# Optimization experiments

Measured on AMD Instinct MI355X. Metric: run time of the kernel, lower is better.

Reference implementation:

```python
import jax, jax.numpy as jnp
import numpy as np
import math

B, S, D, H, N = 4, 2048, 1024, 8, 128  # batch, seq_len, d_model, n_heads, num_osc
ITERS = 10
DT = 0.1
PI = math.pi


def setup_inputs() -> dict:
    key = jax.random.key(0)
    ks = jax.random.split(key, 5)
    return {
        "x": jax.random.normal(ks[0], (B, S, D), jnp.float32),
        "mask": jnp.ones((B, S), jnp.int32),
        "W_phase": jax.random.normal(ks[1], (D, H * N), jnp.float32) / math.sqrt(D),
        "b_phase": jnp.zeros((H * N,), jnp.float32),
        "natural_freq": jax.random.normal(ks[2], (H, N), jnp.float32) * 0.1,
        "coupling": jnp.ones((H, 1, 1), jnp.float32),  # coupling_strength = 1.0
        "W_out": jax.random.normal(ks[3], (H * N, D), jnp.float32) / math.sqrt(H * N),
        "b_out": jnp.zeros((D,), jnp.float32),
    }


def reference(x, mask, W_phase, b_phase, natural_freq, coupling, W_out, b_out):
    # phases: [B, H, S, N]
    ph = (x @ W_phase + b_phase).reshape(B, S, H, N).transpose(0, 2, 1, 3)
    ph = jnp.tanh(ph) * PI
    m = mask.astype(ph.dtype)[:, None, :, None]  # [B,1,S,1] mask over j
    K = coupling.reshape(1, H, 1, 1)
    w = natural_freq.reshape(1, H, 1, N)

    def step(ph, _):
        s = jnp.sin(ph)
        c = jnp.cos(ph)
        # mean_j m_j * sin(theta_i - theta_j) = sin(th_i)*mean(m*cos) - cos(th_i)*mean(m*sin)
        ms = (m * s).mean(axis=2, keepdims=True)  # [B,H,1,N]
        mc = (m * c).mean(axis=2, keepdims=True)
        dtheta = w + K * (s * mc - c * ms)
        ph2 = jnp.mod(ph + DT * dtheta + PI, 2 * PI) - PI
        return ph2, None

    ph, _ = jax.lax.scan(step, ph, None, length=ITERS)
    # from_phase; dropout is identity in eval mode
    y = ph.transpose(0, 2, 1, 3).reshape(B, S, H * N) @ W_out + b_out
    return y
```

## Files before the change

### kernel.cpp

```cpp
#include <hip/hip_runtime.h>
#include <math.h>

#define S_ 2048
#define D_ 1024
#define HN_ 1024
#define B_ 4
#define M_ 8192
#define ITERS_ 10
#define DT_ 0.1f
#define PI_ 3.14159265358979323846f
#define TWOPI_ 6.28318530717958647692f
#define INV2PI_ 0.15915494309189533577f
#define SCALE_ 4096.0f
#define INVSC2_ (1.0f / 16777216.0f)

typedef __attribute__((ext_vector_type(8))) _Float16 f16x8;
typedef __attribute__((ext_vector_type(4))) float f32x4;

__device__ __align__(16) ushort g_xs [(size_t)M_ * 2048];
__device__ __align__(16) ushort g_WpT[(size_t)HN_ * 2048];
__device__ __align__(16) ushort g_WoT[(size_t)D_ * 1024];
__device__ __align__(16) float  g_ph [(size_t)B_ * HN_ * S_];
__device__ __align__(16) ushort g_phh[(size_t)B_ * HN_ * S_];
__device__ __align__(16) ushort g_phT[(size_t)M_ * HN_];

__device__ __forceinline__ ushort f2h(float f) {
    union { _Float16 h; ushort u; } v; v.h = (_Float16)f; return v.u;
}
__device__ __forceinline__ void split2s(float x, ushort& A, ushort& Bc) {
    const float xs = x * SCALE_;
    union { _Float16 h; ushort u; } va, vb;
    va.h = (_Float16)xs;
    const float r = xs - (float)va.h;
    vb.h = (_Float16)r;
    A = va.u; Bc = vb.u;
}
__device__ __forceinline__ void gload16(const void* g, void* l) {
    __builtin_amdgcn_global_load_lds(
        (const __attribute__((address_space(1))) void*)g,
        (__attribute__((address_space(3))) void*)l, 16, 0, 0);
}
__device__ __forceinline__ int pack2(ushort a, ushort b) {
    return (int)(unsigned)a | ((int)(unsigned)b << 16);
}

__global__ __launch_bounds__(256) void split_x(const float* __restrict__ X) {
    const int idx = blockIdx.x * 256 + threadIdx.x;
    const float4 v = ((const float4*)X)[idx];
    const int m  = idx >> 8;
    const int k4 = (idx & 255) * 4;
    ushort a[4], b[4];
    split2s(v.x, a[0], b[0]);
    split2s(v.y, a[1], b[1]);
    split2s(v.z, a[2], b[2]);
    split2s(v.w, a[3], b[3]);
    ushort* row = g_xs + (size_t)m * 2048 + k4;
    int2 oa; oa.x = pack2(a[0], a[1]); oa.y = pack2(a[2], a[3]);
    int2 ob; ob.x = pack2(b[0], b[1]); ob.y = pack2(b[2], b[3]);
    *(int2*)(row)        = oa;
    *(int2*)(row + 1024) = ob;
}

__global__ __launch_bounds__(256) void splitT_Wp(const float* __restrict__ Wp) {
    __shared__ float t[64][68];
    const int k0 = blockIdx.x * 64;
    const int n0 = blockIdx.y * 64;
    const int r = threadIdx.x >> 2;
    const int c = (threadIdx.x & 3) * 16;
    const float* src = Wp + (size_t)(k0 + r) * HN_ + n0 + c;
    #pragma unroll
    for (int q = 0; q < 4; ++q)
        *(float4*)&t[r][c + 4 * q] = ((const float4*)src)[q];
    __syncthreads();
    ushort ha[16], hb[16];
    #pragma unroll
    for (int j = 0; j < 16; ++j)
        split2s(t[c + j][r], ha[j], hb[j]);
    int4 a0, a1, b0, b1;
    a0.x = pack2(ha[0], ha[1]);   a0.y = pack2(ha[2], ha[3]);
    a0.z = pack2(ha[4], ha[5]);   a0.w = pack2(ha[6], ha[7]);
    a1.x = pack2(ha[8], ha[9]);   a1.y = pack2(ha[10], ha[11]);
    a1.z = pack2(ha[12], ha[13]); a1.w = pack2(ha[14], ha[15]);
    b0.x = pack2(hb[0], hb[1]);   b0.y = pack2(hb[2], hb[3]);
    b0.z = pack2(hb[4], hb[5]);   b0.w = pack2(hb[6], hb[7]);
    b1.x = pack2(hb[8], hb[9]);   b1.y = pack2(hb[10], hb[11]);
    b1.z = pack2(hb[12], hb[13]); b1.w = pack2(hb[14], hb[15]);
    ushort* dst = g_WpT + (size_t)(n0 + r) * 2048 + k0 + c;
    *(int4*)(dst)        = a0; *(int4*)(dst + 8)    = a1;
    *(int4*)(dst + 1024) = b0; *(int4*)(dst + 1032) = b1;
}

__global__ __launch_bounds__(256) void castT_Wo(const float* __restrict__ Wo) {
    __shared__ float t[64][68];
    const int k0 = blockIdx.x * 64;
    const int n0 = blockIdx.y * 64;
    const int r = threadIdx.x >> 2;
    const int c = (threadIdx.x & 3) * 16;
    const float* src = Wo + (size_t)(k0 + r) * D_ + n0 + c;
    #pragma unroll
    for (int q = 0; q < 4; ++q)
        *(float4*)&t[r][c + 4 * q] = ((const float4*)src)[q];
    __syncthreads();
    ushort h[16];
    #pragma unroll
    for (int j = 0; j < 16; ++j) h[j] = f2h(t[c + j][r]);
    ushort* dst = g_WoT + (size_t)(n0 + r) * 1024 + k0 + c;
    int4 o0, o1;
    o0.x = pack2(h[0], h[1]);   o0.y = pack2(h[2], h[3]);
    o0.z = pack2(h[4], h[5]);   o0.w = pack2(h[6], h[7]);
    o1.x = pack2(h[8], h[9]);   o1.y = pack2(h[10], h[11]);
    o1.z = pack2(h[12], h[13]); o1.w = pack2(h[14], h[15]);
    *(int4*)dst = o0;
    *(int4*)(dst + 8) = o1;
}

template<int NT, int SPLIT>
__device__ __forceinline__ void gemm_mainloop(const ushort* __restrict__ A,
                                              const ushort* __restrict__ Bm,
                                              ushort* lds,
                                              int m0, int n0, int tid,
                                              f32x4 (&acc)[4][4]) {
    constexpr int KROW = SPLIT ? 2048 : 1024;
    const int l   = tid & 63, wid = tid >> 6;
    const int wm  = wid >> 1, wn = wid & 1;
    const int l15 = l & 15, h = l >> 4;
    const int row4 = tid >> 2;
    const int soff = ((tid & 3) ^ (row4 & 3)) << 4;
    const char* gA = (const char*)(A + (size_t)m0 * KROW);
    const char* gB = (const char*)(Bm + (size_t)n0 * KROW);
    const int rdA = (wm * 64 + l15) * 64 + ((h ^ (l15 & 3)) << 4);
    const int rdB = 8192 + (wn * 64 + l15) * 64 + ((h ^ (l15 & 3)) << 4);

    #define AOFF(T) ((SPLIT && (T) >= 64) ? 2048 + ((T) - 64) * 64 : ((T) & 31) * 64)
    #define BOFF(T) (SPLIT ? ((T) < 32 ? (T) * 64 : ((T) < 64 ? 2048 + ((T) - 32) * 64 \
                                                              : ((T) - 64) * 64)) : (T) * 64)

    #define STAGE(T, BUF) do {                                                    \
        const int ao_ = AOFF(T), bo_ = BOFF(T);                                   \
        char* lb_ = (char*)lds + (BUF) * 16384;                                   \
        gload16(gA + (size_t)(row4)      * (KROW * 2) + ao_ + soff, lb_ + tid * 16);          \
        gload16(gA + (size_t)(row4 + 64) * (KROW * 2) + ao_ + soff, lb_ + 4096 + tid * 16);   \
        gload16(gB + (size_t)(row4)      * (KROW * 2) + bo_ + soff, lb_ + 8192 + tid * 16);   \
        gload16(gB + (size_t)(row4 + 64) * (KROW * 2) + bo_ + soff, lb_ + 12288 + tid * 16);  \
    } while (0)

    #define SB __builtin_amdgcn_sched_barrier(0)

    STAGE(0, 0);

    #pragma unroll 2
    for (int t = 0; t < NT; ++t) {
        SB; __builtin_amdgcn_s_barrier(); SB;
        if (t + 1 < NT) {
            STAGE(t + 1, (t + 1) & 1);
            asm volatile("s_waitcnt vmcnt(4)" ::: "memory");
        } else {
            asm volatile("s_waitcnt vmcnt(0)" ::: "memory");
        }
        SB; __builtin_amdgcn_s_barrier(); SB;

        const char* bb = (const char*)lds + (t & 1) * 16384;
        f16x8 Aa[4], Bb[4];
        #pragma unroll
        for (int i = 0; i < 4; ++i) Aa[i] = *(const f16x8*)(bb + rdA + i * 1024);
        #pragma unroll
        for (int j = 0; j < 4; ++j) Bb[j] = *(const f16x8*)(bb + rdB + j * 1024);
        __builtin_amdgcn_s_setprio(1);
        #pragma unroll
        for (int i = 0; i < 4; ++i)
            #pragma unroll
            for (int j = 0; j < 4; ++j)
                acc[i][j] = __builtin_amdgcn_mfma_f32_16x16x32_f16(
                    Aa[i], Bb[j], acc[i][j], 0, 0, 0);
        __builtin_amdgcn_s_setprio(0);
    }
    #undef STAGE
    #undef SB
    #undef AOFF
    #undef BOFF
}

__device__ __forceinline__ void tile_map(int bid, int& m0, int& n0) {
    const int xcd = bid & 7;
    const int idx = bid >> 3;
    m0 = (xcd * 8 + (idx >> 3)) * 128;
    n0 = (idx & 7) * 128;
}

__global__ __launch_bounds__(256, 4) void gemm1(const float* __restrict__ bias) {
    __shared__ ushort lds[2 * 8192];
    const int tid = threadIdx.x;
    int m0, n0;
    tile_map(blockIdx.x, m0, n0);
    const int wid = tid >> 6, l = tid & 63;
    const int wm = wid >> 1, wn = wid & 1;

    f32x4 acc[4][4];
    #pragma unroll
    for (int i = 0; i < 4; ++i)
        #pragma unroll
        for (int j = 0; j < 4; ++j) acc[i][j] = (f32x4){0.f, 0.f, 0.f, 0.f};

    gemm_mainloop<96, 1>(g_xs, g_WpT, lds, m0, n0, tid, acc);

    const int r4 = (l >> 4) * 4;
    const int cn = l & 15;
    #pragma unroll
    for (int i = 0; i < 4; ++i) {
        const int mg = m0 + wm * 64 + i * 16 + r4;
        const int bidx = mg >> 11;
        const int sg = mg & 2047;
        #pragma unroll
        for (int jj = 0; jj < 4; ++jj) {
            const int ng = n0 + wn * 64 + jj * 16 + cn;
            const float bb = bias[ng];
            float4 o;
            o.x = PI_ * tanhf(fmaf(acc[i][jj][0], INVSC2_, bb));
            o.y = PI_ * tanhf(fmaf(acc[i][jj][1], INVSC2_, bb));
            o.z = PI_ * tanhf(fmaf(acc[i][jj][2], INVSC2_, bb));
            o.w = PI_ * tanhf(fmaf(acc[i][jj][3], INVSC2_, bb));
            *(float4*)(g_ph + ((size_t)bidx * HN_ + ng) * S_ + sg) = o;
        }
    }
}

__global__ __launch_bounds__(256, 4) void gemm3(const float* __restrict__ bias,
                                                float* __restrict__ Y) {
    __shared__ ushort lds[2 * 8192];
    const int tid = threadIdx.x;
    int m0, n0;
    tile_map(blockIdx.x, m0, n0);
    const int wid = tid >> 6, l = tid & 63;
    const int wm = wid >> 1, wn = wid & 1;

    f32x4 acc[4][4];
    #pragma unroll
    for (int i = 0; i < 4; ++i)
        #pragma unroll
        for (int j = 0; j < 4; ++j) acc[i][j] = (f32x4){0.f, 0.f, 0.f, 0.f};

    gemm_mainloop<32, 0>(g_phT, g_WoT, lds, m0, n0, tid, acc);

    const int r4 = (l >> 4) * 4;
    const int cn = l & 15;
    #pragma unroll
    for (int i = 0; i < 4; ++i) {
        const int mg = m0 + wm * 64 + i * 16 + r4;
        #pragma unroll
        for (int jj = 0; jj < 4; ++jj) {
            const int ng = n0 + wn * 64 + jj * 16 + cn;
            const float bb = bias[ng];
            #pragma unroll
            for (int r = 0; r < 4; ++r)
                Y[(size_t)(mg + r) * D_ + ng] = acc[i][jj][r] + bb;
        }
    }
}

__global__ __launch_bounds__(256) void kuramoto(const int* __restrict__ mask,
                                                const float* __restrict__ natf,
                                                const float* __restrict__ coup) {
    const int wave = blockIdx.x * 4 + (threadIdx.x >> 6);
    const int lane = threadIdx.x & 63;
    const int b = wave >> 10;
    const int hn = wave & 1023;
    const int h = hn >> 7;

    const float wf = natf[hn];
    const float K = coup[h];

    const float* base = g_ph + ((size_t)b * HN_ + hn) * S_;

    float ph[32];
    #pragma unroll
    for (int i = 0; i < 8; ++i) {
        float4 v = *(const float4*)(base + i * 256 + lane * 4);
        ph[4 * i + 0] = v.x; ph[4 * i + 1] = v.y;
        ph[4 * i + 2] = v.z; ph[4 * i + 3] = v.w;
    }

    const int* mb = mask + b * S_;
    unsigned mbits = 0;
    #pragma unroll
    for (int i = 0; i < 8; ++i) {
        int4 mv = *(const int4*)(mb + i * 256 + lane * 4);
        mbits |= (mv.x != 0 ? 1u : 0u) << (4 * i + 0);
        mbits |= (mv.y != 0 ? 1u : 0u) << (4 * i + 1);
        mbits |= (mv.z != 0 ? 1u : 0u) << (4 * i + 2);
        mbits |= (mv.w != 0 ? 1u : 0u) << (4 * i + 3);
    }

    for (int it = 0; it < ITERS_; ++it) {
        float s[32], c[32];
        float ls = 0.f, lc = 0.f;
        #pragma unroll
        for (int i = 0; i < 32; ++i) {
            s[i] = __sinf(ph[i]);
            c[i] = __cosf(ph[i]);
            const float mf = (float)((mbits >> i) & 1u);
            ls = fmaf(mf, s[i], ls);
            lc = fmaf(mf, c[i], lc);
        }
        #pragma unroll
        for (int off = 32; off; off >>= 1) {
            ls += __shfl_xor(ls, off);
            lc += __shfl_xor(lc, off);
        }
        const float ms = ls * (1.f / 2048.f);
        const float mc = lc * (1.f / 2048.f);
        #pragma unroll
        for (int i = 0; i < 32; ++i) {
            const float dth = fmaf(K, fmaf(s[i], mc, -c[i] * ms), wf);
            float t = fmaf(DT_, dth, ph[i]) + PI_;
            t -= TWOPI_ * floorf(t * INV2PI_);
            ph[i] = t - PI_;
        }
    }

    ushort* ob = g_phh + ((size_t)b * HN_ + hn) * S_;
    #pragma unroll
    for (int i = 0; i < 8; ++i) {
        ushort4 o;
        o.x = f2h(ph[4 * i + 0]); o.y = f2h(ph[4 * i + 1]);
        o.z = f2h(ph[4 * i + 2]); o.w = f2h(ph[4 * i + 3]);
        *(ushort4*)(ob + i * 256 + lane * 4) = o;
    }
}

__global__ __launch_bounds__(256) void transpose_ph() {
    __shared__ ushort t[64][72];
    const int b = blockIdx.z;
    const int h0 = blockIdx.y * 64;
    const int s0 = blockIdx.x * 64;
    const int r = threadIdx.x >> 2;
    const int c = (threadIdx.x & 3) * 16;
    const ushort* src = g_phh + ((size_t)b * HN_ + h0 + r) * S_ + s0 + c;
    *(int4*)&t[r][c] = *(const int4*)src;
    *(int4*)&t[r][c + 8] = *(const int4*)(src + 8);
    __syncthreads();
    ushort o[16];
    #pragma unroll
    for (int j = 0; j < 16; ++j) o[j] = t[c + j][r];
    ushort* dst = g_phT + ((size_t)(b * S_ + s0 + r)) * HN_ + h0 + c;
    int4 o0, o1;
    o0.x = pack2(o[0], o[1]);   o0.y = pack2(o[2], o[3]);
    o0.z = pack2(o[4], o[5]);   o0.w = pack2(o[6], o[7]);
    o1.x = pack2(o[8], o[9]);   o1.y = pack2(o[10], o[11]);
    o1.z = pack2(o[12], o[13]); o1.w = pack2(o[14], o[15]);
    *(int4*)dst = o0;
    *(int4*)(dst + 8) = o1;
}

extern "C" void kernel_launch(void* const* d_in, const int* in_sizes, int n_in,
                              void* d_out, int out_size, void* d_ws, size_t ws_size,
                              hipStream_t stream) {
    const float* x    = (const float*)d_in[0];
    const int*   mask = (const int*)d_in[1];
    const float* Wp   = (const float*)d_in[2];
    const float* bp   = (const float*)d_in[3];
    const float* natf = (const float*)d_in[4];
    const float* coup = (const float*)d_in[5];
    const float* Wo   = (const float*)d_in[6];
    const float* bo   = (const float*)d_in[7];
    float* y = (float*)d_out;

    split_x  <<<dim3(8192),         256, 0, stream>>>(x);
    splitT_Wp<<<dim3(16, 16),       256, 0, stream>>>(Wp);
    castT_Wo <<<dim3(16, 16),       256, 0, stream>>>(Wo);
    gemm1    <<<dim3(512),          256, 0, stream>>>(bp);
    kuramoto <<<dim3(1024),         256, 0, stream>>>(mask, natf, coup);
    transpose_ph<<<dim3(32, 16, 4), 256, 0, stream>>>();
    gemm3    <<<dim3(512),          256, 0, stream>>>(bo, y);
}
```

Before: 192.6 us.

## Retile GEMMs to 128x64 blocks with 8 waves and 64-wide K stages

Both GEMM kernels move from 128x128 tiles with 4 waves (each wave computing 64x64) to 128x64 tiles with 8 waves (each wave computing 32x32). Each stage now loads a K-slice of 64 instead of 32, with a new XOR swizzle for shared memory, and the launch grids double to 1024 blocks of 512 threads. The goal is more waves and blocks in flight to raise occupancy and hide latency. In exchange each wave gets less register-level reuse, and B tiles are reloaded more often across the grid.

```diff
diff --git a/kernel.cpp b/kernel.cpp
--- a/kernel.cpp
+++ b/kernel.cpp
@@ -119,29 +119,38 @@
                                               const ushort* __restrict__ Bm,
                                               ushort* lds,
                                               int m0, int n0, int tid,
-                                              f32x4 (&acc)[4][4]) {
+                                              f32x4 (&acc)[2][2]) {
     constexpr int KROW = SPLIT ? 2048 : 1024;
-    const int l   = tid & 63, wid = tid >> 6;
-    const int wm  = wid >> 1, wn = wid & 1;
-    const int l15 = l & 15, h = l >> 4;
-    const int row4 = tid >> 2;
-    const int soff = ((tid & 3) ^ (row4 & 3)) << 4;
+    const int l = tid & 63, wid = tid >> 6;
+    const int wm = wid >> 1, wn = wid & 1;
+    const int r8   = l >> 3;
+    const int swzo = ((l & 7) * 16) ^ (r8 << 4);
     const char* gA = (const char*)(A + (size_t)m0 * KROW);
     const char* gB = (const char*)(Bm + (size_t)n0 * KROW);
-    const int rdA = (wm * 64 + l15) * 64 + ((h ^ (l15 & 3)) << 4);
-    const int rdB = 8192 + (wn * 64 + l15) * 64 + ((h ^ (l15 & 3)) << 4);
-
-    #define AOFF(T) ((SPLIT && (T) >= 64) ? 2048 + ((T) - 64) * 64 : ((T) & 31) * 64)
-    #define BOFF(T) (SPLIT ? ((T) < 32 ? (T) * 64 : ((T) < 64 ? 2048 + ((T) - 32) * 64 \
-                                                              : ((T) - 64) * 64)) : (T) * 64)
-
-    #define STAGE(T, BUF) do {                                                    \
-        const int ao_ = AOFF(T), bo_ = BOFF(T);                                   \
-        char* lb_ = (char*)lds + (BUF) * 16384;                                   \
-        gload16(gA + (size_t)(row4)      * (KROW * 2) + ao_ + soff, lb_ + tid * 16);          \
-        gload16(gA + (size_t)(row4 + 64) * (KROW * 2) + ao_ + soff, lb_ + 4096 + tid * 16);   \
-        gload16(gB + (size_t)(row4)      * (KROW * 2) + bo_ + soff, lb_ + 8192 + tid * 16);   \
-        gload16(gB + (size_t)(row4 + 64) * (KROW * 2) + bo_ + soff, lb_ + 12288 + tid * 16);  \
+
+    const int l15 = l & 15;
+    const int xk  = (l15 & 7) << 4;
+    const int sl0 = (((l >> 4) * 16)) ^ xk;
+    const int sl1 = (64 + ((l >> 4) * 16)) ^ xk;
+    const char* pA = (const char*)lds + (wm * 32 + l15) * 128;
+    const char* pB = (const char*)lds + 16384 + (wn * 32 + l15) * 128;
+
+    #define AOFF(T) ((size_t)(SPLIT ? ((T) < 32 ? ((T) & 15) * 128 : 2048 + ((T) - 32) * 128) \
+                                    : (T) * 128))
+    #define BOFF(T) ((size_t)(SPLIT ? ((T) < 16 ? (T) * 128                                   \
+                                     : ((T) < 32 ? 2048 + ((T) - 16) * 128                    \
+                                                 : ((T) - 32) * 128))                         \
+                                    : (T) * 128))
+
+    #define STAGE(T, BUF) do {                                                     \
+        const size_t ao_ = AOFF(T) + swzo, bo_ = BOFF(T) + swzo;                   \
+        char* lb_ = (char*)lds + (BUF) * 24576;                                    \
+        gload16(gA + (size_t)(wid * 16 + r8)     * (KROW * 2) + ao_,               \
+                lb_ + wid * 2048);                                                 \
+        gload16(gA + (size_t)(wid * 16 + 8 + r8) * (KROW * 2) + ao_,               \
+                lb_ + wid * 2048 + 1024);                                          \
+        gload16(gB + (size_t)(wid * 8 + r8)      * (KROW * 2) + bo_,               \
+                lb_ + 16384 + wid * 1024);                                         \
     } while (0)
 
     #define SB __builtin_amdgcn_sched_barrier(0)
@@ -153,25 +162,33 @@
         SB; __builtin_amdgcn_s_barrier(); SB;
         if (t + 1 < NT) {
             STAGE(t + 1, (t + 1) & 1);
-            asm volatile("s_waitcnt vmcnt(4)" ::: "memory");
+            asm volatile("s_waitcnt vmcnt(3)" ::: "memory");
         } else {
             asm volatile("s_waitcnt vmcnt(0)" ::: "memory");
         }
         SB; __builtin_amdgcn_s_barrier(); SB;
 
-        const char* bb = (const char*)lds + (t & 1) * 16384;
-        f16x8 Aa[4], Bb[4];
-        #pragma unroll
-        for (int i = 0; i < 4; ++i) Aa[i] = *(const f16x8*)(bb + rdA + i * 1024);
-        #pragma unroll
-        for (int j = 0; j < 4; ++j) Bb[j] = *(const f16x8*)(bb + rdB + j * 1024);
+        const int bo = (t & 1) * 24576;
+        f16x8 Aa[2][2], Bb[2][2];
+        #pragma unroll
+        for (int i = 0; i < 2; ++i) {
+            Aa[i][0] = *(const f16x8*)(pA + bo + i * 2048 + sl0);
+            Aa[i][1] = *(const f16x8*)(pA + bo + i * 2048 + sl1);
+        }
+        #pragma unroll
+        for (int j = 0; j < 2; ++j) {
+            Bb[j][0] = *(const f16x8*)(pB + bo + j * 2048 + sl0);
+            Bb[j][1] = *(const f16x8*)(pB + bo + j * 2048 + sl1);
+        }
         __builtin_amdgcn_s_setprio(1);
         #pragma unroll
-        for (int i = 0; i < 4; ++i)
+        for (int ks = 0; ks < 2; ++ks)
             #pragma unroll
-            for (int j = 0; j < 4; ++j)
-                acc[i][j] = __builtin_amdgcn_mfma_f32_16x16x32_f16(
-                    Aa[i], Bb[j], acc[i][j], 0, 0, 0);
+            for (int i = 0; i < 2; ++i)
+                #pragma unroll
+                for (int j = 0; j < 2; ++j)
+                    acc[i][j] = __builtin_amdgcn_mfma_f32_16x16x32_f16(
+                        Aa[i][ks], Bb[j][ks], acc[i][j], 0, 0, 0);
         __builtin_amdgcn_s_setprio(0);
     }
     #undef STAGE
@@ -183,36 +200,36 @@
 __device__ __forceinline__ void tile_map(int bid, int& m0, int& n0) {
     const int xcd = bid & 7;
     const int idx = bid >> 3;
-    m0 = (xcd * 8 + (idx >> 3)) * 128;
-    n0 = (idx & 7) * 128;
-}
-
-__global__ __launch_bounds__(256, 4) void gemm1(const float* __restrict__ bias) {
-    __shared__ ushort lds[2 * 8192];
+    m0 = (xcd * 8 + (idx >> 4)) * 128;
+    n0 = (idx & 15) * 64;
+}
+
+__global__ __launch_bounds__(512, 6) void gemm1(const float* __restrict__ bias) {
+    __shared__ ushort lds[2 * 12288];
     const int tid = threadIdx.x;
     int m0, n0;
     tile_map(blockIdx.x, m0, n0);
     const int wid = tid >> 6, l = tid & 63;
     const int wm = wid >> 1, wn = wid & 1;
 
-    f32x4 acc[4][4];
-    #pragma unroll
-    for (int i = 0; i < 4; ++i)
-        #pragma unroll
-        for (int j = 0; j < 4; ++j) acc[i][j] = (f32x4){0.f, 0.f, 0.f, 0.f};
-
-    gemm_mainloop<96, 1>(g_xs, g_WpT, lds, m0, n0, tid, acc);
+    f32x4 acc[2][2];
+    #pragma unroll
+    for (int i = 0; i < 2; ++i)
+        #pragma unroll
+        for (int j = 0; j < 2; ++j) acc[i][j] = (f32x4){0.f, 0.f, 0.f, 0.f};
+
+    gemm_mainloop<48, 1>(g_xs, g_WpT, lds, m0, n0, tid, acc);
 
     const int r4 = (l >> 4) * 4;
     const int cn = l & 15;
     #pragma unroll
-    for (int i = 0; i < 4; ++i) {
-        const int mg = m0 + wm * 64 + i * 16 + r4;
+    for (int i = 0; i < 2; ++i) {
+        const int mg = m0 + wm * 32 + i * 16 + r4;
         const int bidx = mg >> 11;
         const int sg = mg & 2047;
         #pragma unroll
-        for (int jj = 0; jj < 4; ++jj) {
-            const int ng = n0 + wn * 64 + jj * 16 + cn;
+        for (int jj = 0; jj < 2; ++jj) {
+            const int ng = n0 + wn * 32 + jj * 16 + cn;
             const float bb = bias[ng];
             float4 o;
             o.x = PI_ * tanhf(fmaf(acc[i][jj][0], INVSC2_, bb));
@@ -224,31 +241,31 @@
     }
 }
 
-__global__ __launch_bounds__(256, 4) void gemm3(const float* __restrict__ bias,
+__global__ __launch_bounds__(512, 6) void gemm3(const float* __restrict__ bias,
                                                 float* __restrict__ Y) {
-    __shared__ ushort lds[2 * 8192];
+    __shared__ ushort lds[2 * 12288];
     const int tid = threadIdx.x;
     int m0, n0;
     tile_map(blockIdx.x, m0, n0);
     const int wid = tid >> 6, l = tid & 63;
     const int wm = wid >> 1, wn = wid & 1;
 
-    f32x4 acc[4][4];
-    #pragma unroll
-    for (int i = 0; i < 4; ++i)
-        #pragma unroll
-        for (int j = 0; j < 4; ++j) acc[i][j] = (f32x4){0.f, 0.f, 0.f, 0.f};
-
-    gemm_mainloop<32, 0>(g_phT, g_WoT, lds, m0, n0, tid, acc);
+    f32x4 acc[2][2];
+    #pragma unroll
+    for (int i = 0; i < 2; ++i)
+        #pragma unroll
+        for (int j = 0; j < 2; ++j) acc[i][j] = (f32x4){0.f, 0.f, 0.f, 0.f};
+
+    gemm_mainloop<16, 0>(g_phT, g_WoT, lds, m0, n0, tid, acc);
 
     const int r4 = (l >> 4) * 4;
     const int cn = l & 15;
     #pragma unroll
-    for (int i = 0; i < 4; ++i) {
-        const int mg = m0 + wm * 64 + i * 16 + r4;
-        #pragma unroll
-        for (int jj = 0; jj < 4; ++jj) {
-            const int ng = n0 + wn * 64 + jj * 16 + cn;
+    for (int i = 0; i < 2; ++i) {
+        const int mg = m0 + wm * 32 + i * 16 + r4;
+        #pragma unroll
+        for (int jj = 0; jj < 2; ++jj) {
+            const int ng = n0 + wn * 32 + jj * 16 + cn;
             const float bb = bias[ng];
             #pragma unroll
             for (int r = 0; r < 4; ++r)
@@ -367,8 +384,8 @@
     split_x  <<<dim3(8192),         256, 0, stream>>>(x);
     splitT_Wp<<<dim3(16, 16),       256, 0, stream>>>(Wp);
     castT_Wo <<<dim3(16, 16),       256, 0, stream>>>(Wo);
-    gemm1    <<<dim3(512),          256, 0, stream>>>(bp);
+    gemm1    <<<dim3(1024),         512, 0, stream>>>(bp);
     kuramoto <<<dim3(1024),         256, 0, stream>>>(mask, natf, coup);
     transpose_ph<<<dim3(32, 16, 4), 256, 0, stream>>>();
-    gemm3    <<<dim3(512),          256, 0, stream>>>(bo, y);
-}
+    gemm3    <<<dim3(1024),         512, 0, stream>>>(bo, y);
+}
```

After: 189.2 us. No clear change (-1.8%).
